# Kernel optimization log

Hardware: AMD Instinct MI355X
Metric: run time of the kernel (lower is better)

Reference implementation:

```python
import jax, jax.numpy as jnp
import numpy as np

NUM_HEADS = 8


def setup_inputs() -> dict:
    key = jax.random.key(0)
    ks = jax.random.split(key, 16)
    B, C = 4, 512
    size = (8, 16, 16)
    def w(k):
        return jax.random.normal(k, (C, C), dtype=jnp.float32) * 0.02
    z = lambda: jnp.zeros((C,), jnp.float32)
    return {
        'x1': jax.random.normal(ks[0], (B, C) + size, dtype=jnp.float32),
        'x2': jax.random.normal(ks[1], (B, C) + size, dtype=jnp.float32),
        'Wq': w(ks[2]), 'bq': z(),
        'Wk': w(ks[3]), 'bk': z(),
        'Wv1': w(ks[4]), 'bv1': z(),
        'Wv2': w(ks[5]), 'bv2': z(),
        'Wo1': w(ks[6]), 'bo1': z(),
        'Wo2': w(ks[7]), 'bo2': z(),
    }


def reference(x1, x2, Wq, bq, Wk, bk, Wv1, bv1, Wv2, bv2, Wo1, bo1, Wo2, bo2):
    B, C = x1.shape[:2]
    size = x1.shape[2:]              # spatial dims, e.g. (8,16,16)
    N = int(np.prod(size))           # tokens
    dh = C // NUM_HEADS
    # flatten spatial -> (B, N, C)
    h1 = x1.reshape(B, C, N).transpose(0, 2, 1)
    h2 = x2.reshape(B, C, N).transpose(0, 2, 1)

    def heads(x):                    # (B,N,C) -> (B,H,N,dh)
        return x.reshape(B, N, NUM_HEADS, dh).transpose(0, 2, 1, 3)

    q = heads(h1 @ Wq + bq)
    k = heads(h2 @ Wk + bk)
    v1 = heads(h1 @ Wv1 + bv1)
    v2 = heads(h2 @ Wv2 + bv2)

    scores = jnp.einsum('bhqd,bhkd->bhqk', q, k) / jnp.sqrt(jnp.float32(dh))
    p1 = jax.nn.softmax(scores, axis=-2)                      # normalize over queries
    p2 = jnp.swapaxes(jax.nn.softmax(scores, axis=-1), -1, -2)  # (B,H,Nk,Nq)

    ctx1 = jnp.einsum('bhqk,bhkd->bhqd', p1, v1)
    ctx2 = jnp.einsum('bhkq,bhqd->bhkd', p2, v2)

    def merge(ctx):                  # (B,H,N,dh) -> (B,N,C)
        return ctx.transpose(0, 2, 1, 3).reshape(B, N, C)

    o1 = (merge(ctx1) @ Wo1 + bo1).transpose(0, 2, 1).reshape((B, C) + size) + x1
    o2 = (merge(ctx2) @ Wo2 + bo2).transpose(0, 2, 1).reshape((B, C) + size) + x2
    return (o1, o2)
```

## Files before the change

### kernel.cpp

```cpp
#include <hip/hip_runtime.h>

typedef __attribute__((ext_vector_type(8))) __bf16 bf16x8;
typedef __attribute__((ext_vector_type(4))) float f32x4;
typedef __attribute__((ext_vector_type(16))) float f32x16;
typedef unsigned int u32;

#define MFMA32(a, b, c) __builtin_amdgcn_mfma_f32_32x32x16_bf16((a), (b), (c), 0, 0, 0)
#define EXP2(x) __builtin_amdgcn_exp2f(x)

static constexpr int Bsz = 4, C = 512, N = 2048, H = 8, DH = 64;
static constexpr int BN = Bsz * N;
static constexpr size_t BCN = (size_t)Bsz * C * N;
static constexpr float SM_C = 0.18033688011112042f;

__device__ __forceinline__ void gload16(const void* g, void* lds) {
  __builtin_amdgcn_global_load_lds(
      (const __attribute__((address_space(1))) u32*)g,
      (__attribute__((address_space(3))) u32*)lds, 16, 0, 0);
}

__device__ __forceinline__ u32 cvt_pk_bf16(float lo, float hi) {
  u32 r;
  asm("v_cvt_pk_bf16_f32 %0, %1, %2" : "=v"(r) : "v"(lo), "v"(hi));
  return r;
}

__device__ __forceinline__ void permswap32(u32& a, u32& b) {
  asm volatile("v_permlane32_swap_b32 %0, %1" : "+v"(a), "+v"(b));
}

static constexpr size_t SZ_BF = (size_t)BN * C * sizeof(__bf16);
static constexpr size_t SZ_W  = (size_t)C * C * sizeof(__bf16);
static constexpr size_t SZ_ST = (size_t)Bsz * H * N * sizeof(float);
static constexpr size_t OFF_HT1  = 0;
static constexpr size_t OFF_HT2  = OFF_HT1 + SZ_BF;
static constexpr size_t OFF_Q    = OFF_HT2 + SZ_BF;
static constexpr size_t OFF_K    = OFF_Q + SZ_BF;
static constexpr size_t OFF_VT1  = OFF_K + SZ_BF;
static constexpr size_t OFF_VT2  = OFF_VT1 + SZ_BF;
static constexpr size_t OFF_CTX1 = OFF_VT2 + SZ_BF;
static constexpr size_t OFF_CTX2 = OFF_CTX1 + SZ_BF;
static constexpr size_t OFF_WQT  = OFF_CTX2 + SZ_BF;
static constexpr size_t OFF_WKT  = OFF_WQT + SZ_W;
static constexpr size_t OFF_WV1T = OFF_WKT + SZ_W;
static constexpr size_t OFF_WV2T = OFF_WV1T + SZ_W;
static constexpr size_t OFF_WO1T = OFF_WV2T + SZ_W;
static constexpr size_t OFF_WO2T = OFF_WO1T + SZ_W;
static constexpr size_t OFF_QRS  = OFF_WO2T + SZ_W;
static constexpr size_t OFF_KRS  = OFF_QRS + SZ_ST;

__global__ __launch_bounds__(256) void k_tc2(const float* __restrict__ x1,
                                             const float* __restrict__ x2,
                                             __bf16* __restrict__ h1,
                                             __bf16* __restrict__ h2) {
  __shared__ __bf16 tile[64][66];
  int z = blockIdx.z;
  size_t boff = (size_t)(z & 3) * C * N;
  const float* src = (z < 4 ? x1 : x2) + boff;
  __bf16* dst = (z < 4 ? h1 : h2) + boff;
  int r0 = blockIdx.y * 64, c0 = blockIdx.x * 64;
  int t = threadIdx.x;
  int cl = t & 63, rr = t >> 6;
#pragma unroll
  for (int i = 0; i < 16; ++i) {
    int r = rr * 16 + i;
    tile[r][cl] = (__bf16)src[(size_t)(r0 + r) * N + c0 + cl];
  }
  __syncthreads();
#pragma unroll
  for (int i = 0; i < 16; ++i) {
    int c = rr * 16 + i;
    dst[(size_t)(c0 + c) * C + r0 + cl] = tile[cl][c];
  }
}

struct WT6 {
  const float* src[6];
  __bf16* dst[6];
};
__global__ __launch_bounds__(256) void k_tcw(WT6 p) {
  __shared__ __bf16 tile[64][66];
  int z = blockIdx.z;
  const float* src = p.src[z];
  __bf16* dst = p.dst[z];
  int r0 = blockIdx.y * 64, c0 = blockIdx.x * 64;
  int t = threadIdx.x;
  int cl = t & 63, rr = t >> 6;
#pragma unroll
  for (int i = 0; i < 16; ++i) {
    int r = rr * 16 + i;
    tile[r][cl] = (__bf16)src[(size_t)(r0 + r) * C + c0 + cl];
  }
  __syncthreads();
#pragma unroll
  for (int i = 0; i < 16; ++i) {
    int c = rr * 16 + i;
    dst[(size_t)(c0 + c) * C + r0 + cl] = tile[cl][c];
  }
}

struct GArgs {
  const __bf16* A; const __bf16* Bt; const float* bias; const float* rs;
  __bf16* outb; float* outf; const float* resid; float scale;
};

template <int MODE>
__global__ __launch_bounds__(256, 2) void k_gemm(GArgs g0, GArgs g1) {
  __shared__ __bf16 As[2 * 128 * 64];
  __shared__ __bf16 Bs[2 * 128 * 64];
  int lin = blockIdx.x;
  int swz = (lin & 7) * 64 + (lin >> 3);
  int dir = swz >> 8;
  int inner = swz & 255;
  const __bf16* Ap = dir ? g1.A : g0.A;
  const __bf16* Bp = dir ? g1.Bt : g0.Bt;
  const float* bias = dir ? g1.bias : g0.bias;
  const float* rs = dir ? g1.rs : g0.rs;
  __bf16* outb = dir ? g1.outb : g0.outb;
  float* outf = dir ? g1.outf : g0.outf;
  const float* resid = dir ? g1.resid : g0.resid;
  float scale = dir ? g1.scale : g0.scale;
  int m0 = (inner & 63) * 128, n0 = (inner >> 6) * 128;
  int t = threadIdx.x, lane = t & 63, w = t >> 6;
  int wm = w >> 1, wn = w & 1;
  int l31 = lane & 31, hi = lane >> 5;
  int srow = t >> 3;
  int sc8 = ((t & 7) ^ (srow & 7)) * 8;
  int swA = (l31 & 7) << 4;
  f32x16 acc[2][2] = {};

#define GSTAGE(p, k0)                                                        \
  {                                                                          \
    _Pragma("unroll") for (int gI = 0; gI < 4; ++gI) {                       \
      int row_ = gI * 32 + srow;                                             \
      gload16(&Ap[(size_t)(m0 + row_) * C + (k0) + sc8],                     \
              (char*)As + (p) * 16384 + gI * 4096 + w * 1024);               \
      gload16(&Bp[(size_t)(n0 + row_) * C + (k0) + sc8],                     \
              (char*)Bs + (p) * 16384 + gI * 4096 + w * 1024);               \
    }                                                                        \
  }

  GSTAGE(0, 0)
  __syncthreads();
  for (int ks = 0; ks < 8; ++ks) {
    int p = ks & 1;
    if (ks < 7) GSTAGE(p ^ 1, (ks + 1) * 64)
    const char* ab = (const char*)As + p * 16384;
    const char* bb = (const char*)Bs + p * 16384;
#pragma unroll
    for (int kk = 0; kk < 4; ++kk) {
      int ko = (kk * 32 + hi * 16);
      bf16x8 a0 = *(const bf16x8*)(ab + (wm * 64 + l31) * 128 + (ko ^ swA));
      bf16x8 a1 = *(const bf16x8*)(ab + (wm * 64 + 32 + l31) * 128 + (ko ^ swA));
      bf16x8 b0 = *(const bf16x8*)(bb + (wn * 64 + l31) * 128 + (ko ^ swA));
      bf16x8 b1 = *(const bf16x8*)(bb + (wn * 64 + 32 + l31) * 128 + (ko ^ swA));
      acc[0][0] = MFMA32(a0, b0, acc[0][0]);
      acc[0][1] = MFMA32(a0, b1, acc[0][1]);
      acc[1][0] = MFMA32(a1, b0, acc[1][0]);
      acc[1][1] = MFMA32(a1, b1, acc[1][1]);
    }
    __syncthreads();
  }
#pragma unroll
  for (int mi = 0; mi < 2; ++mi)
#pragma unroll
    for (int ni = 0; ni < 2; ++ni) {
      int gn = n0 + wn * 64 + ni * 32 + l31;
      float bv = bias[gn];
#pragma unroll
      for (int g2 = 0; g2 < 4; ++g2) {
        int gm = m0 + wm * 64 + mi * 32 + 8 * g2 + 4 * hi;
        int b = gm >> 11, n = gm & 2047;
        if (MODE == 0) {
          int h = gn >> 6, d = gn & 63;
          size_t base = (size_t)(b * 8 + h) * 2048 + n;
#pragma unroll
          for (int j = 0; j < 4; ++j)
            outb[(base + j) * 64 + d] = (__bf16)((acc[mi][ni][4 * g2 + j] + bv) * scale);
        } else if (MODE == 1) {
          int h = gn >> 6, d = gn & 63;
          size_t tok = (size_t)(b * 8 + h) * 2048 + n;
          float4 rv = *reinterpret_cast<const float4*>(&rs[tok]);
          size_t addr = ((size_t)(b * 8 + h) * 64 + d) * 2048 + n;
          union { __bf16 h4[4]; uint2 u; } pk;
          pk.h4[0] = (__bf16)((acc[mi][ni][4 * g2 + 0] + bv) * rv.x);
          pk.h4[1] = (__bf16)((acc[mi][ni][4 * g2 + 1] + bv) * rv.y);
          pk.h4[2] = (__bf16)((acc[mi][ni][4 * g2 + 2] + bv) * rv.z);
          pk.h4[3] = (__bf16)((acc[mi][ni][4 * g2 + 3] + bv) * rv.w);
          *reinterpret_cast<uint2*>(&outb[addr]) = pk.u;
        } else {
          size_t addr = ((size_t)b * C + gn) * 2048 + n;
          float4 xv = *reinterpret_cast<const float4*>(&resid[addr]);
          float4 ov;
          ov.x = acc[mi][ni][4 * g2 + 0] + bv + xv.x;
          ov.y = acc[mi][ni][4 * g2 + 1] + bv + xv.y;
          ov.z = acc[mi][ni][4 * g2 + 2] + bv + xv.z;
          ov.w = acc[mi][ni][4 * g2 + 3] + bv + xv.w;
          *reinterpret_cast<float4*>(&outf[addr]) = ov;
        }
      }
    }
}

struct SArgs { const __bf16* X; const __bf16* Y; float* ors; };

__global__ __launch_bounds__(256, 2) void k_stats(SArgs sa0, SArgs sa1) {
  __shared__ __bf16 Ys[2 * 64 * 64];
  int lin = blockIdx.x;
  int swz = (lin & 7) * 64 + (lin >> 3);
  int dir = swz >> 8;
  int inner = swz & 255;
  const __bf16* X = dir ? sa1.X : sa0.X;
  const __bf16* Y = dir ? sa1.Y : sa0.Y;
  float* ors = dir ? sa1.ors : sa0.ors;
  int bh = inner >> 3, xblk = inner & 7;
  int t = threadIdx.x, lane = t & 63, w = t >> 6;
  int l31 = lane & 31, hi = lane >> 5;
  const __bf16* Xb = X + (size_t)bh * N * DH;
  const __bf16* Yb = Y + (size_t)bh * N * DH;
  int qg = xblk * 256 + w * 64 + l31;
  bf16x8 xq[2][4];
#pragma unroll
  for (int s = 0; s < 2; ++s)
#pragma unroll
    for (int kk = 0; kk < 4; ++kk)
      xq[s][kk] = *(const bf16x8*)&Xb[(size_t)(qg + s * 32) * DH + kk * 16 + hi * 8];
  int srow = t >> 3;
  int sc8 = ((t & 7) ^ (srow & 7)) * 8;
#define SSTAGE(p, kc2)                                                       \
  {                                                                          \
    char* yb_ = (char*)Ys + (p) * 8192 + w * 1024;                           \
    gload16(&Yb[(size_t)((kc2) + srow) * DH + sc8], yb_);                    \
    gload16(&Yb[(size_t)((kc2) + 32 + srow) * DH + sc8], yb_ + 4096);        \
  }
  float sum0 = 0.f, sum1 = 0.f;
  SSTAGE(0, 0)
  __syncthreads();
  for (int it = 0; it < 32; ++it) {
    int p = it & 1;
    if (it < 31) SSTAGE(p ^ 1, (it + 1) * 64)
    const char* yb = (const char*)Ys + p * 8192;
#pragma unroll
    for (int cblk = 0; cblk < 2; ++cblk) {
      f32x16 s0 = {}, s1 = {};
      int row = cblk * 32 + l31;
      int sw = (row & 7) << 4;
#pragma unroll
      for (int kk = 0; kk < 4; ++kk) {
        bf16x8 yf = *(const bf16x8*)(yb + row * 128 + ((kk * 32 + hi * 16) ^ sw));
        s0 = MFMA32(yf, xq[0][kk], s0);
        s1 = MFMA32(yf, xq[1][kk], s1);
      }
#pragma unroll
      for (int e = 0; e < 16; ++e) {
        sum0 += EXP2(s0[e]);
        sum1 += EXP2(s1[e]);
      }
    }
    __syncthreads();
  }
  sum0 += __shfl_xor(sum0, 32, 64);
  sum1 += __shfl_xor(sum1, 32, 64);
  if (hi == 0) {
    ors[(size_t)bh * N + qg] = 1.0f / sum0;
    ors[(size_t)bh * N + qg + 32] = 1.0f / sum1;
  }
}

struct CArgs { const __bf16* X; const __bf16* Y; const __bf16* Vt; __bf16* out; };

__global__ __launch_bounds__(256, 2) void k_ctx(CArgs c0, CArgs c1) {
  __shared__ __bf16 Ys[2 * 64 * 64];
  __shared__ __bf16 Vs[2 * 64 * 64];
  int lin = blockIdx.x;
  int swz = (lin & 7) * 64 + (lin >> 3);
  int dir = swz >> 8;
  int inner = swz & 255;
  const __bf16* X = dir ? c1.X : c0.X;
  const __bf16* Y = dir ? c1.Y : c0.Y;
  const __bf16* Vt = dir ? c1.Vt : c0.Vt;
  __bf16* out = dir ? c1.out : c0.out;
  int bh = inner >> 3, xblk = inner & 7;
  int b = bh >> 3, h = bh & 7;
  int t = threadIdx.x, lane = t & 63, w = t >> 6;
  int l31 = lane & 31, hi = lane >> 5;
  const __bf16* Xb = X + (size_t)bh * N * DH;
  const __bf16* Yb = Y + (size_t)bh * N * DH;
  const __bf16* Vb = Vt + (size_t)bh * DH * N;
  int qg = xblk * 256 + w * 64 + l31;
  bf16x8 xq[2][4];
#pragma unroll
  for (int s = 0; s < 2; ++s)
#pragma unroll
    for (int kk = 0; kk < 4; ++kk)
      xq[s][kk] = *(const bf16x8*)&Xb[(size_t)(qg + s * 32) * DH + kk * 16 + hi * 8];
  int srow = t >> 3;
  int sc8 = ((t & 7) ^ (srow & 7)) * 8;
#define CSTAGE(p, kc2)                                                       \
  {                                                                          \
    char* yb_ = (char*)Ys + (p) * 8192 + w * 1024;                           \
    char* vb_ = (char*)Vs + (p) * 8192 + w * 1024;                           \
    gload16(&Yb[(size_t)((kc2) + srow) * DH + sc8], yb_);                    \
    gload16(&Yb[(size_t)((kc2) + 32 + srow) * DH + sc8], yb_ + 4096);        \
    gload16(&Vb[(size_t)srow * N + (kc2) + sc8], vb_);                       \
    gload16(&Vb[(size_t)(32 + srow) * N + (kc2) + sc8], vb_ + 4096);         \
  }
  f32x16 oacc[2][2] = {};
  CSTAGE(0, 0)
  __syncthreads();
  for (int it = 0; it < 32; ++it) {
    int p = it & 1;
    if (it < 31) CSTAGE(p ^ 1, (it + 1) * 64)
    const char* yb = (const char*)Ys + p * 8192;
    const char* vb = (const char*)Vs + p * 8192;
    u32 wl[2][2][4], wh[2][2][4];
#pragma unroll
    for (int cblk = 0; cblk < 2; ++cblk) {
      f32x16 s0 = {}, s1 = {};
      int row = cblk * 32 + l31;
      int sw = (row & 7) << 4;
#pragma unroll
      for (int kk = 0; kk < 4; ++kk) {
        bf16x8 yf = *(const bf16x8*)(yb + row * 128 + ((kk * 32 + hi * 16) ^ sw));
        s0 = MFMA32(yf, xq[0][kk], s0);
        s1 = MFMA32(yf, xq[1][kk], s1);
      }
#pragma unroll
      for (int g = 0; g < 4; ++g) {
        wl[0][cblk][g] = cvt_pk_bf16(EXP2(s0[4 * g + 0]), EXP2(s0[4 * g + 1]));
        wh[0][cblk][g] = cvt_pk_bf16(EXP2(s0[4 * g + 2]), EXP2(s0[4 * g + 3]));
        wl[1][cblk][g] = cvt_pk_bf16(EXP2(s1[4 * g + 0]), EXP2(s1[4 * g + 1]));
        wh[1][cblk][g] = cvt_pk_bf16(EXP2(s1[4 * g + 2]), EXP2(s1[4 * g + 3]));
      }
    }
#pragma unroll
    for (int ct = 0; ct < 4; ++ct) {
      int cb = ct >> 1, sh = ct & 1;
      u32 p00 = wl[0][cb][2 * sh], p01 = wl[0][cb][2 * sh + 1];
      u32 p02 = wh[0][cb][2 * sh], p03 = wh[0][cb][2 * sh + 1];
      permswap32(p00, p01);
      permswap32(p02, p03);
      union { u32 wd[4]; bf16x8 v; } pf0;
      pf0.wd[0] = p00; pf0.wd[1] = p02; pf0.wd[2] = p01; pf0.wd[3] = p03;
      u32 p10 = wl[1][cb][2 * sh], p11 = wl[1][cb][2 * sh + 1];
      u32 p12 = wh[1][cb][2 * sh], p13 = wh[1][cb][2 * sh + 1];
      permswap32(p10, p11);
      permswap32(p12, p13);
      union { u32 wd[4]; bf16x8 v; } pf1;
      pf1.wd[0] = p10; pf1.wd[1] = p12; pf1.wd[2] = p11; pf1.wd[3] = p13;
#pragma unroll
      for (int dblk = 0; dblk < 2; ++dblk) {
        int vrow = dblk * 32 + l31;
        int vw = (vrow & 7) << 4;
        bf16x8 vf = *(const bf16x8*)(vb + vrow * 128 + ((ct * 32 + hi * 16) ^ vw));
        oacc[0][dblk] = MFMA32(vf, pf0.v, oacc[0][dblk]);
        oacc[1][dblk] = MFMA32(vf, pf1.v, oacc[1][dblk]);
      }
    }
    __syncthreads();
  }
#pragma unroll
  for (int s = 0; s < 2; ++s)
#pragma unroll
    for (int dblk = 0; dblk < 2; ++dblk)
#pragma unroll
      for (int g = 0; g < 4; ++g) {
        union { __bf16 h4[4]; uint2 u; } pk;
#pragma unroll
        for (int m = 0; m < 4; ++m) pk.h4[m] = (__bf16)oacc[s][dblk][4 * g + m];
        int d = dblk * 32 + 8 * g + 4 * hi;
        size_t addr = ((size_t)b * N + qg + s * 32) * C + h * 64 + d;
        *reinterpret_cast<uint2*>(&out[addr]) = pk.u;
      }
}

extern "C" void kernel_launch(void* const* d_in, const int* in_sizes, int n_in,
                              void* d_out, int out_size, void* d_ws, size_t ws_size,
                              hipStream_t stream) {
  (void)in_sizes; (void)n_in; (void)out_size; (void)ws_size;
  const float* x1  = (const float*)d_in[0];
  const float* x2  = (const float*)d_in[1];
  const float* Wq  = (const float*)d_in[2];
  const float* bq  = (const float*)d_in[3];
  const float* Wk  = (const float*)d_in[4];
  const float* bk  = (const float*)d_in[5];
  const float* Wv1 = (const float*)d_in[6];
  const float* bv1 = (const float*)d_in[7];
  const float* Wv2 = (const float*)d_in[8];
  const float* bv2 = (const float*)d_in[9];
  const float* Wo1 = (const float*)d_in[10];
  const float* bo1 = (const float*)d_in[11];
  const float* Wo2 = (const float*)d_in[12];
  const float* bo2 = (const float*)d_in[13];

  char* ws = (char*)d_ws;
  __bf16* ht1  = (__bf16*)(ws + OFF_HT1);
  __bf16* ht2  = (__bf16*)(ws + OFF_HT2);
  __bf16* qb   = (__bf16*)(ws + OFF_Q);
  __bf16* kb   = (__bf16*)(ws + OFF_K);
  __bf16* vt1  = (__bf16*)(ws + OFF_VT1);
  __bf16* vt2  = (__bf16*)(ws + OFF_VT2);
  __bf16* ctx1 = (__bf16*)(ws + OFF_CTX1);
  __bf16* ctx2 = (__bf16*)(ws + OFF_CTX2);
  __bf16* wqt  = (__bf16*)(ws + OFF_WQT);
  __bf16* wkt  = (__bf16*)(ws + OFF_WKT);
  __bf16* wv1t = (__bf16*)(ws + OFF_WV1T);
  __bf16* wv2t = (__bf16*)(ws + OFF_WV2T);
  __bf16* wo1t = (__bf16*)(ws + OFF_WO1T);
  __bf16* wo2t = (__bf16*)(ws + OFF_WO2T);
  float* qrs = (float*)(ws + OFF_QRS);
  float* krs = (float*)(ws + OFF_KRS);
  float* outf = (float*)d_out;

  dim3 blk(256);
  k_tc2<<<dim3(32, 8, 8), blk, 0, stream>>>(x1, x2, ht1, ht2);
  WT6 wt;
  wt.src[0] = Wq;  wt.dst[0] = wqt;
  wt.src[1] = Wk;  wt.dst[1] = wkt;
  wt.src[2] = Wv1; wt.dst[2] = wv1t;
  wt.src[3] = Wv2; wt.dst[3] = wv2t;
  wt.src[4] = Wo1; wt.dst[4] = wo1t;
  wt.src[5] = Wo2; wt.dst[5] = wo2t;
  k_tcw<<<dim3(8, 8, 6), blk, 0, stream>>>(wt);

  GArgs gq0{ht1, wqt, bq, nullptr, qb, nullptr, nullptr, SM_C};
  GArgs gq1{ht2, wkt, bk, nullptr, kb, nullptr, nullptr, 1.0f};
  k_gemm<0><<<512, blk, 0, stream>>>(gq0, gq1);

  SArgs st0{qb, kb, qrs};
  SArgs st1{kb, qb, krs};
  k_stats<<<512, blk, 0, stream>>>(st0, st1);

  GArgs gv0{ht1, wv1t, bv1, krs, vt1, nullptr, nullptr, 0.f};
  GArgs gv1{ht2, wv2t, bv2, qrs, vt2, nullptr, nullptr, 0.f};
  k_gemm<1><<<512, blk, 0, stream>>>(gv0, gv1);

  CArgs cc0{qb, kb, vt1, ctx1};
  CArgs cc1{kb, qb, vt2, ctx2};
  k_ctx<<<512, blk, 0, stream>>>(cc0, cc1);

  GArgs go0{ctx1, wo1t, bo1, nullptr, nullptr, outf, x1, 0.f};
  GArgs go1{ctx2, wo2t, bo2, nullptr, nullptr, outf + BCN, x2, 0.f};
  k_gemm<2><<<512, blk, 0, stream>>>(go0, go1);
}
```

Before: 192.9 us.

## Compute row and column softmax sums in one score pass with atomics

The stats kernel now computes QK^T once and gathers both the per-query row sums and, through cross-lane shuffles and atomicAdd, the per-key column sums. Before, it computed the scores twice, once per direction. Each block handles half of the key range, and a zero kernel clears the accumulators first. The V-projection GEMM now takes reciprocals of the raw sums itself. Separately, the context kernel switches to 128-key tiles with wider swizzled LDS staging, and both kernels raise wave priority around their MFMA blocks. The risks are atomic contention on the key sums, extra shuffle work, and larger LDS use that may reduce occupancy.

Result: slower. 342.1 us (+77.4%).

```diff
diff --git a/kernel.cpp b/kernel.cpp
--- a/kernel.cpp
+++ b/kernel.cpp
@@ -7,6 +7,7 @@
 
 #define MFMA32(a, b, c) __builtin_amdgcn_mfma_f32_32x32x16_bf16((a), (b), (c), 0, 0, 0)
 #define EXP2(x) __builtin_amdgcn_exp2f(x)
+#define SETPRIO(n) __builtin_amdgcn_s_setprio(n)
 
 static constexpr int Bsz = 4, C = 512, N = 2048, H = 8, DH = 64;
 static constexpr int BN = Bsz * N;
@@ -46,8 +47,12 @@
 static constexpr size_t OFF_WV2T = OFF_WV1T + SZ_W;
 static constexpr size_t OFF_WO1T = OFF_WV2T + SZ_W;
 static constexpr size_t OFF_WO2T = OFF_WO1T + SZ_W;
-static constexpr size_t OFF_QRS  = OFF_WO2T + SZ_W;
-static constexpr size_t OFF_KRS  = OFF_QRS + SZ_ST;
+static constexpr size_t OFF_QS   = OFF_WO2T + SZ_W;
+static constexpr size_t OFF_KS   = OFF_QS + SZ_ST;
+
+__global__ __launch_bounds__(256) void k_zero(float* __restrict__ p) {
+  p[(size_t)blockIdx.x * 256 + threadIdx.x] = 0.f;
+}
 
 __global__ __launch_bounds__(256) void k_tc2(const float* __restrict__ x1,
                                              const float* __restrict__ x2,
@@ -180,13 +185,13 @@
         } else if (MODE == 1) {
           int h = gn >> 6, d = gn & 63;
           size_t tok = (size_t)(b * 8 + h) * 2048 + n;
-          float4 rv = *reinterpret_cast<const float4*>(&rs[tok]);
+          float4 sv = *reinterpret_cast<const float4*>(&rs[tok]);
           size_t addr = ((size_t)(b * 8 + h) * 64 + d) * 2048 + n;
           union { __bf16 h4[4]; uint2 u; } pk;
-          pk.h4[0] = (__bf16)((acc[mi][ni][4 * g2 + 0] + bv) * rv.x);
-          pk.h4[1] = (__bf16)((acc[mi][ni][4 * g2 + 1] + bv) * rv.y);
-          pk.h4[2] = (__bf16)((acc[mi][ni][4 * g2 + 2] + bv) * rv.z);
-          pk.h4[3] = (__bf16)((acc[mi][ni][4 * g2 + 3] + bv) * rv.w);
+          pk.h4[0] = (__bf16)((acc[mi][ni][4 * g2 + 0] + bv) * __builtin_amdgcn_rcpf(sv.x));
+          pk.h4[1] = (__bf16)((acc[mi][ni][4 * g2 + 1] + bv) * __builtin_amdgcn_rcpf(sv.y));
+          pk.h4[2] = (__bf16)((acc[mi][ni][4 * g2 + 2] + bv) * __builtin_amdgcn_rcpf(sv.z));
+          pk.h4[3] = (__bf16)((acc[mi][ni][4 * g2 + 3] + bv) * __builtin_amdgcn_rcpf(sv.w));
           *reinterpret_cast<uint2*>(&outb[addr]) = pk.u;
         } else {
           size_t addr = ((size_t)b * C + gn) * 2048 + n;
@@ -202,76 +207,90 @@
     }
 }
 
-struct SArgs { const __bf16* X; const __bf16* Y; float* ors; };
-
-__global__ __launch_bounds__(256, 2) void k_stats(SArgs sa0, SArgs sa1) {
+__global__ __launch_bounds__(256, 2) void k_stats(
+    const __bf16* __restrict__ Q, const __bf16* __restrict__ K,
+    float* __restrict__ qs, float* __restrict__ ks) {
   __shared__ __bf16 Ys[2 * 64 * 64];
   int lin = blockIdx.x;
   int swz = (lin & 7) * 64 + (lin >> 3);
-  int dir = swz >> 8;
-  int inner = swz & 255;
-  const __bf16* X = dir ? sa1.X : sa0.X;
-  const __bf16* Y = dir ? sa1.Y : sa0.Y;
-  float* ors = dir ? sa1.ors : sa0.ors;
-  int bh = inner >> 3, xblk = inner & 7;
+  int bh = swz >> 4, qblk = (swz >> 1) & 7, kh = swz & 1;
   int t = threadIdx.x, lane = t & 63, w = t >> 6;
   int l31 = lane & 31, hi = lane >> 5;
-  const __bf16* Xb = X + (size_t)bh * N * DH;
-  const __bf16* Yb = Y + (size_t)bh * N * DH;
-  int qg = xblk * 256 + w * 64 + l31;
+  const __bf16* Qb = Q + (size_t)bh * N * DH;
+  const __bf16* Kb = K + (size_t)bh * N * DH;
+  int qg = qblk * 256 + w * 64 + l31;
   bf16x8 xq[2][4];
 #pragma unroll
   for (int s = 0; s < 2; ++s)
 #pragma unroll
     for (int kk = 0; kk < 4; ++kk)
-      xq[s][kk] = *(const bf16x8*)&Xb[(size_t)(qg + s * 32) * DH + kk * 16 + hi * 8];
+      xq[s][kk] = *(const bf16x8*)&Qb[(size_t)(qg + s * 32) * DH + kk * 16 + hi * 8];
   int srow = t >> 3;
   int sc8 = ((t & 7) ^ (srow & 7)) * 8;
+  int kbase = kh * 1024;
 #define SSTAGE(p, kc2)                                                       \
   {                                                                          \
     char* yb_ = (char*)Ys + (p) * 8192 + w * 1024;                           \
-    gload16(&Yb[(size_t)((kc2) + srow) * DH + sc8], yb_);                    \
-    gload16(&Yb[(size_t)((kc2) + 32 + srow) * DH + sc8], yb_ + 4096);        \
-  }
-  float sum0 = 0.f, sum1 = 0.f;
-  SSTAGE(0, 0)
+    gload16(&Kb[(size_t)((kc2) + srow) * DH + sc8], yb_);                    \
+    gload16(&Kb[(size_t)((kc2) + 32 + srow) * DH + sc8], yb_ + 4096);        \
+  }
+  float qsum0 = 0.f, qsum1 = 0.f;
+  SSTAGE(0, kbase)
   __syncthreads();
-  for (int it = 0; it < 32; ++it) {
+  for (int it = 0; it < 16; ++it) {
     int p = it & 1;
-    if (it < 31) SSTAGE(p ^ 1, (it + 1) * 64)
+    if (it < 15) SSTAGE(p ^ 1, kbase + (it + 1) * 64)
     const char* yb = (const char*)Ys + p * 8192;
 #pragma unroll
     for (int cblk = 0; cblk < 2; ++cblk) {
       f32x16 s0 = {}, s1 = {};
       int row = cblk * 32 + l31;
       int sw = (row & 7) << 4;
+      SETPRIO(1);
 #pragma unroll
       for (int kk = 0; kk < 4; ++kk) {
         bf16x8 yf = *(const bf16x8*)(yb + row * 128 + ((kk * 32 + hi * 16) ^ sw));
         s0 = MFMA32(yf, xq[0][kk], s0);
         s1 = MFMA32(yf, xq[1][kk], s1);
       }
+      SETPRIO(0);
+      float r[16];
 #pragma unroll
       for (int e = 0; e < 16; ++e) {
-        sum0 += EXP2(s0[e]);
-        sum1 += EXP2(s1[e]);
+        float p0 = EXP2(s0[e]);
+        float p1 = EXP2(s1[e]);
+        qsum0 += p0;
+        qsum1 += p1;
+        r[e] = p0 + p1;
+      }
+#pragma unroll
+      for (int m = 1; m <= 16; m <<= 1)
+#pragma unroll
+        for (int e = 0; e < 16; ++e) r[e] += __shfl_xor(r[e], m, 64);
+      if (l31 == 0) {
+        int kc = kbase + it * 64 + cblk * 32;
+#pragma unroll
+        for (int e = 0; e < 16; ++e) {
+          int krow = kc + 8 * (e >> 2) + 4 * hi + (e & 3);
+          atomicAdd(&ks[(size_t)bh * N + krow], r[e]);
+        }
       }
     }
     __syncthreads();
   }
-  sum0 += __shfl_xor(sum0, 32, 64);
-  sum1 += __shfl_xor(sum1, 32, 64);
+  qsum0 += __shfl_xor(qsum0, 32, 64);
+  qsum1 += __shfl_xor(qsum1, 32, 64);
   if (hi == 0) {
-    ors[(size_t)bh * N + qg] = 1.0f / sum0;
-    ors[(size_t)bh * N + qg + 32] = 1.0f / sum1;
+    atomicAdd(&qs[(size_t)bh * N + qg], qsum0);
+    atomicAdd(&qs[(size_t)bh * N + qg + 32], qsum1);
   }
 }
 
 struct CArgs { const __bf16* X; const __bf16* Y; const __bf16* Vt; __bf16* out; };
 
 __global__ __launch_bounds__(256, 2) void k_ctx(CArgs c0, CArgs c1) {
-  __shared__ __bf16 Ys[2 * 64 * 64];
-  __shared__ __bf16 Vs[2 * 64 * 64];
+  __shared__ __bf16 Ys[2 * 128 * 64];
+  __shared__ __bf16 Vs[2 * 64 * 128];
   int lin = blockIdx.x;
   int swz = (lin & 7) * 64 + (lin >> 3);
   int dir = swz >> 8;
@@ -296,65 +315,73 @@
       xq[s][kk] = *(const bf16x8*)&Xb[(size_t)(qg + s * 32) * DH + kk * 16 + hi * 8];
   int srow = t >> 3;
   int sc8 = ((t & 7) ^ (srow & 7)) * 8;
-#define CSTAGE(p, kc2)                                                       \
-  {                                                                          \
-    char* yb_ = (char*)Ys + (p) * 8192 + w * 1024;                           \
-    char* vb_ = (char*)Vs + (p) * 8192 + w * 1024;                           \
-    gload16(&Yb[(size_t)((kc2) + srow) * DH + sc8], yb_);                    \
-    gload16(&Yb[(size_t)((kc2) + 32 + srow) * DH + sc8], yb_ + 4096);        \
-    gload16(&Vb[(size_t)srow * N + (kc2) + sc8], vb_);                       \
-    gload16(&Vb[(size_t)(32 + srow) * N + (kc2) + sc8], vb_ + 4096);         \
+  int vrow_s = t >> 4;
+  int vc8 = ((t & 15) ^ (vrow_s & 15)) * 8;
+#define CSTAGE(p, kc2)                                                        \
+  {                                                                           \
+    char* yb_ = (char*)Ys + (p) * 16384 + w * 1024;                           \
+    char* vb_ = (char*)Vs + (p) * 16384 + w * 1024;                           \
+    _Pragma("unroll") for (int gI = 0; gI < 4; ++gI) {                        \
+      gload16(&Yb[(size_t)((kc2) + gI * 32 + srow) * DH + sc8],               \
+              yb_ + gI * 4096);                                               \
+      gload16(&Vb[(size_t)(gI * 16 + vrow_s) * N + (kc2) + vc8],              \
+              vb_ + gI * 4096);                                               \
+    }                                                                         \
   }
   f32x16 oacc[2][2] = {};
   CSTAGE(0, 0)
   __syncthreads();
-  for (int it = 0; it < 32; ++it) {
+  for (int it = 0; it < 16; ++it) {
     int p = it & 1;
-    if (it < 31) CSTAGE(p ^ 1, (it + 1) * 64)
-    const char* yb = (const char*)Ys + p * 8192;
-    const char* vb = (const char*)Vs + p * 8192;
-    u32 wl[2][2][4], wh[2][2][4];
-#pragma unroll
-    for (int cblk = 0; cblk < 2; ++cblk) {
+    if (it < 15) CSTAGE(p ^ 1, (it + 1) * 128)
+    const char* yb = (const char*)Ys + p * 16384;
+    const char* vb = (const char*)Vs + p * 16384;
+#pragma unroll
+    for (int cblk = 0; cblk < 4; ++cblk) {
       f32x16 s0 = {}, s1 = {};
       int row = cblk * 32 + l31;
       int sw = (row & 7) << 4;
+      SETPRIO(1);
 #pragma unroll
       for (int kk = 0; kk < 4; ++kk) {
         bf16x8 yf = *(const bf16x8*)(yb + row * 128 + ((kk * 32 + hi * 16) ^ sw));
         s0 = MFMA32(yf, xq[0][kk], s0);
         s1 = MFMA32(yf, xq[1][kk], s1);
       }
+      SETPRIO(0);
+      u32 wl0[4], wh0[4], wl1[4], wh1[4];
 #pragma unroll
       for (int g = 0; g < 4; ++g) {
-        wl[0][cblk][g] = cvt_pk_bf16(EXP2(s0[4 * g + 0]), EXP2(s0[4 * g + 1]));
-        wh[0][cblk][g] = cvt_pk_bf16(EXP2(s0[4 * g + 2]), EXP2(s0[4 * g + 3]));
-        wl[1][cblk][g] = cvt_pk_bf16(EXP2(s1[4 * g + 0]), EXP2(s1[4 * g + 1]));
-        wh[1][cblk][g] = cvt_pk_bf16(EXP2(s1[4 * g + 2]), EXP2(s1[4 * g + 3]));
-      }
-    }
-#pragma unroll
-    for (int ct = 0; ct < 4; ++ct) {
-      int cb = ct >> 1, sh = ct & 1;
-      u32 p00 = wl[0][cb][2 * sh], p01 = wl[0][cb][2 * sh + 1];
-      u32 p02 = wh[0][cb][2 * sh], p03 = wh[0][cb][2 * sh + 1];
-      permswap32(p00, p01);
-      permswap32(p02, p03);
-      union { u32 wd[4]; bf16x8 v; } pf0;
-      pf0.wd[0] = p00; pf0.wd[1] = p02; pf0.wd[2] = p01; pf0.wd[3] = p03;
-      u32 p10 = wl[1][cb][2 * sh], p11 = wl[1][cb][2 * sh + 1];
-      u32 p12 = wh[1][cb][2 * sh], p13 = wh[1][cb][2 * sh + 1];
-      permswap32(p10, p11);
-      permswap32(p12, p13);
-      union { u32 wd[4]; bf16x8 v; } pf1;
-      pf1.wd[0] = p10; pf1.wd[1] = p12; pf1.wd[2] = p11; pf1.wd[3] = p13;
-#pragma unroll
-      for (int dblk = 0; dblk < 2; ++dblk) {
-        int vrow = dblk * 32 + l31;
-        int vw = (vrow & 7) << 4;
-        bf16x8 vf = *(const bf16x8*)(vb + vrow * 128 + ((ct * 32 + hi * 16) ^ vw));
-        oacc[0][dblk] = MFMA32(vf, pf0.v, oacc[0][dblk]);
-        oacc[1][dblk] = MFMA32(vf, pf1.v, oacc[1][dblk]);
+        wl0[g] = cvt_pk_bf16(EXP2(s0[4 * g + 0]), EXP2(s0[4 * g + 1]));
+        wh0[g] = cvt_pk_bf16(EXP2(s0[4 * g + 2]), EXP2(s0[4 * g + 3]));
+        wl1[g] = cvt_pk_bf16(EXP2(s1[4 * g + 0]), EXP2(s1[4 * g + 1]));
+        wh1[g] = cvt_pk_bf16(EXP2(s1[4 * g + 2]), EXP2(s1[4 * g + 3]));
+      }
+#pragma unroll
+      for (int sh = 0; sh < 2; ++sh) {
+        int ct = cblk * 2 + sh;
+        u32 p00 = wl0[2 * sh], p01 = wl0[2 * sh + 1];
+        u32 p02 = wh0[2 * sh], p03 = wh0[2 * sh + 1];
+        permswap32(p00, p01);
+        permswap32(p02, p03);
+        union { u32 wd[4]; bf16x8 v; } pf0;
+        pf0.wd[0] = p00; pf0.wd[1] = p02; pf0.wd[2] = p01; pf0.wd[3] = p03;
+        u32 p10 = wl1[2 * sh], p11 = wl1[2 * sh + 1];
+        u32 p12 = wh1[2 * sh], p13 = wh1[2 * sh + 1];
+        permswap32(p10, p11);
+        permswap32(p12, p13);
+        union { u32 wd[4]; bf16x8 v; } pf1;
+        pf1.wd[0] = p10; pf1.wd[1] = p12; pf1.wd[2] = p11; pf1.wd[3] = p13;
+        SETPRIO(1);
+#pragma unroll
+        for (int dblk = 0; dblk < 2; ++dblk) {
+          int vrow = dblk * 32 + l31;
+          int vw = (vrow & 15) << 4;
+          bf16x8 vf = *(const bf16x8*)(vb + vrow * 256 + ((ct * 32 + hi * 16) ^ vw));
+          oacc[0][dblk] = MFMA32(vf, pf0.v, oacc[0][dblk]);
+          oacc[1][dblk] = MFMA32(vf, pf1.v, oacc[1][dblk]);
+        }
+        SETPRIO(0);
       }
     }
     __syncthreads();
@@ -408,11 +435,13 @@
   __bf16* wv2t = (__bf16*)(ws + OFF_WV2T);
   __bf16* wo1t = (__bf16*)(ws + OFF_WO1T);
   __bf16* wo2t = (__bf16*)(ws + OFF_WO2T);
-  float* qrs = (float*)(ws + OFF_QRS);
-  float* krs = (float*)(ws + OFF_KRS);
+  float* qs = (float*)(ws + OFF_QS);
+  float* ks = (float*)(ws + OFF_KS);
   float* outf = (float*)d_out;
 
   dim3 blk(256);
+  k_zero<<<512, blk, 0, stream>>>(qs);
+
   k_tc2<<<dim3(32, 8, 8), blk, 0, stream>>>(x1, x2, ht1, ht2);
   WT6 wt;
   wt.src[0] = Wq;  wt.dst[0] = wqt;
@@ -427,12 +456,10 @@
   GArgs gq1{ht2, wkt, bk, nullptr, kb, nullptr, nullptr, 1.0f};
   k_gemm<0><<<512, blk, 0, stream>>>(gq0, gq1);
 
-  SArgs st0{qb, kb, qrs};
-  SArgs st1{kb, qb, krs};
-  k_stats<<<512, blk, 0, stream>>>(st0, st1);
-
-  GArgs gv0{ht1, wv1t, bv1, krs, vt1, nullptr, nullptr, 0.f};
-  GArgs gv1{ht2, wv2t, bv2, qrs, vt2, nullptr, nullptr, 0.f};
+  k_stats<<<512, blk, 0, stream>>>(qb, kb, qs, ks);
+
+  GArgs gv0{ht1, wv1t, bv1, ks, vt1, nullptr, nullptr, 0.f};
+  GArgs gv1{ht2, wv2t, bv2, qs, vt2, nullptr, nullptr, 0.f};
   k_gemm<1><<<512, blk, 0, stream>>>(gv0, gv1);
 
   CArgs cc0{qb, kb, vt1, ctx1};
```
